# Performance work log

Hardware: AMD Instinct MI355X
Metric: run time of the kernel (lower is better)

## Reference

```python
import jax, jax.numpy as jnp
import numpy as np

B, T, D = 256, 512, 8      # batch, seq_len, Feature_number
H = 120                    # hidden_size
L = 4                      # layers=['s','s','s','s']
NH = D                     # num_heads = Feature_number
HD = H // NH               # head dim = 15
EPS = 1e-5


def setup_inputs() -> dict:
    key = jax.random.key(0)
    ks = jax.random.split(key, 16)
    rn = lambda k, shape, s=0.1: (jax.random.normal(k, shape, jnp.float32) * s)
    return {
        "x":   jax.random.normal(ks[0], (B, T, D), jnp.float32),
        # input->gate weights, stacked over layers
        "Wi":  rn(ks[1], (L, H, D)),
        "Wf":  rn(ks[2], (L, H, D)),
        "Wz":  rn(ks[3], (L, H, D)),
        "Wo":  rn(ks[4], (L, H, D)),
        # block-diagonal (multi-head) recurrent weights: [L, NH, HD, HD]
        "Ri":  rn(ks[5], (L, NH, HD, HD)),
        "Rf":  rn(ks[6], (L, NH, HD, HD)),
        "Rz":  rn(ks[7], (L, NH, HD, HD)),
        "Ro":  rn(ks[8], (L, NH, HD, HD)),
        "bi":  rn(ks[9],  (L, H), 0.02),
        "bf":  rn(ks[10], (L, H), 0.02),
        "bz":  rn(ks[11], (L, H), 0.02),
        "bo":  rn(ks[12], (L, H), 0.02),
        # per-block down-projection back to Feature_number (residual block)
        "Wp":  rn(ks[13], (L, D, H)),
        "bp":  jnp.zeros((L, D), jnp.float32),
        # BatchNorm1d(Feature_number) affine params
        "gamma": jnp.ones((D,), jnp.float32),
        "beta":  jnp.zeros((D,), jnp.float32),
        # fc5: Linear(Feature_number, 1)
        "Wfc": rn(ks[14], (1, D)),
        "bfc": jnp.zeros((1,), jnp.float32),
    }


def _slstm_layer(x, Wi, Wf, Wz, Wo, Ri, Rf, Rz, Ro, bi, bf, bz, bo, Wp, bp):
    """One sLSTM block: exp-gated recurrence with stabilizer, then down-proj + residual.
    x: [B, T, D] -> [B, T, D]."""
    Bn = x.shape[0]

    def rec(h, R):  # block-diagonal recurrent matmul: [B,H] x [NH,HD,HD] -> [B,H]
        return jnp.einsum("bnd,nde->bne", h.reshape(Bn, NH, HD), R).reshape(Bn, H)

    def step(carry, x_t):
        h, c, n, m = carry                       # each [B, H]
        it = x_t @ Wi.T + rec(h, Ri) + bi        # input gate pre-act
        ft = x_t @ Wf.T + rec(h, Rf) + bf        # forget gate pre-act (exp gating)
        z = jnp.tanh(x_t @ Wz.T + rec(h, Rz) + bz)
        o = jax.nn.sigmoid(x_t @ Wo.T + rec(h, Ro) + bo)
        m_new = jnp.maximum(ft + m, it)          # stabilizer state
        i_p = jnp.exp(it - m_new)
        f_p = jnp.exp(ft + m - m_new)
        c_new = f_p * c + i_p * z
        n_new = f_p * n + i_p                    # normalizer state
        h_new = o * (c_new / n_new)
        return (h_new, c_new, n_new, m_new), h_new

    z0 = jnp.zeros((Bn, H), x.dtype)
    (_, _, _, _), hs = jax.lax.scan(step, (z0, z0, z0, z0), jnp.swapaxes(x, 0, 1))
    y = jnp.einsum("tbh,dh->tbd", hs, Wp) + bp   # down-project to D
    return x + jnp.swapaxes(y, 0, 1)             # residual


def reference(x, Wi, Wf, Wz, Wo, Ri, Rf, Rz, Ro, bi, bf, bz, bo, Wp, bp,
              gamma, beta, Wfc, bfc):
    h = x
    for l in range(L):
        h = _slstm_layer(h, Wi[l], Wf[l], Wz[l], Wo[l], Ri[l], Rf[l], Rz[l], Ro[l],
                         bi[l], bf[l], bz[l], bo[l], Wp[l], bp[l])
    last = h[:, -1, :]                            # [B, D]
    # BatchNorm1d in training mode (batch stats, biased variance)
    mu = jnp.mean(last, axis=0)
    var = jnp.mean((last - mu) ** 2, axis=0)
    bn = (last - mu) / jnp.sqrt(var + EPS) * gamma + beta
    out = jax.nn.sigmoid(bn @ Wfc.T + bfc)        # [B, 1]
    return out[:, 0]                              # squeeze(1) -> [B]
```

## Files before the change

### kernel.cpp

```cpp
#include <hip/hip_runtime.h>
#include <math.h>

#define Bsz 256
#define T   512
#define Dd  8
#define Hh  120
#define Ll  4
#define NHn 8
#define HDd 15
#define HP  16
#define EPSf 1e-5f

__device__ __forceinline__ float fast_rcp(float x) {
#if __has_builtin(__builtin_amdgcn_rcpf)
    return __builtin_amdgcn_rcpf(x);
#else
    return 1.f / x;
#endif
}
__device__ __forceinline__ float tanh_fast(float x) {
    float e = __expf(2.f * x);
    return 1.f - 2.f * fast_rcp(e + 1.f);
}
__device__ __forceinline__ float sigm_fast(float x) {
    return fast_rcp(1.f + __expf(-x));
}

__global__ __launch_bounds__(512, 2) void slstm_kernel(
    const float* __restrict__ x,
    const float* __restrict__ Wi, const float* __restrict__ Wf,
    const float* __restrict__ Wz, const float* __restrict__ Wo,
    const float* __restrict__ Ri, const float* __restrict__ Rf,
    const float* __restrict__ Rz, const float* __restrict__ Ro,
    const float* __restrict__ bi, const float* __restrict__ bf,
    const float* __restrict__ bz, const float* __restrict__ bo,
    const float* __restrict__ Wp, const float* __restrict__ bp,
    float* __restrict__ last_out)
{
    __shared__ __align__(16) float xs[T * Dd];
    __shared__ __align__(16) float hb[Ll][2][NHn * HP];

    const int tid = threadIdx.x;
    const int b   = blockIdx.x;
    const int l   = tid >> 7;
    const int j   = tid & 127;

    {
        const float4* xg  = (const float4*)(x + (size_t)b * T * Dd);
        float4*       xs4 = (float4*)xs;
        xs4[tid]       = xg[tid];
        xs4[tid + 512] = xg[tid + 512];
        ((float*)hb)[tid]       = 0.f;
        ((float*)hb)[tid + 512] = 0.f;
    }

    const bool gl = (j < Hh);
    const int jj  = gl ? j : 0;
    const int n   = jj / HDd;
    const int e   = jj - n * HDd;
    float wI[Dd], wF[Dd], wZ[Dd], wO[Dd];
    float rI[HDd], rF[HDd], rZ[HDd], rO[HDd];
    {
        const int row = (l * Hh + jj) * Dd;
#pragma unroll
        for (int d = 0; d < Dd; ++d) {
            wI[d] = Wi[row + d]; wF[d] = Wf[row + d];
            wZ[d] = Wz[row + d]; wO[d] = Wo[row + d];
        }
        const int rb = ((l * NHn + n) * HDd) * HDd + e;
#pragma unroll
        for (int d = 0; d < HDd; ++d) {
            rI[d] = Ri[rb + d * HDd]; rF[d] = Rf[rb + d * HDd];
            rZ[d] = Rz[rb + d * HDd]; rO[d] = Ro[rb + d * HDd];
        }
    }
    float bI = bi[l * Hh + jj], bF = bf[l * Hh + jj];
    float bZ = bz[l * Hh + jj], bO = bo[l * Hh + jj];

    const int p  = (j >= 64) ? (j - 64) : j;
    const int d8 = p & 7, ch = p >> 3;
    float wp_r[16];
    {
        const int base = l * Dd * Hh + d8 * Hh + ch * HDd;
#pragma unroll
        for (int k = 0; k < HDd; ++k) wp_r[k] = Wp[base + k];
        wp_r[15] = 0.f;
    }
    float bp_r = bp[l * Dd + d8];

#pragma unroll
    for (int d = 0; d < Dd; ++d)
        asm volatile("" : "+v"(wI[d]), "+v"(wF[d]), "+v"(wZ[d]), "+v"(wO[d]));
#pragma unroll
    for (int d = 0; d < HDd; ++d)
        asm volatile("" : "+v"(rI[d]), "+v"(rF[d]), "+v"(rZ[d]), "+v"(rO[d]));
#pragma unroll
    for (int k = 0; k < 16; ++k)
        asm volatile("" : "+v"(wp_r[k]));
    asm volatile("" : "+v"(bI), "+v"(bF), "+v"(bZ), "+v"(bO));
    asm volatile("" : "+v"(bp_r));

    float cst = 0.f, nst = 0.f, mst = 0.f;

    __syncthreads();

    for (int tau = 0; tau < T + 2 * Ll - 1; ++tau) {
        const int t_g = tau - 2 * l;
        const int t_p = t_g - 1;

        if (gl && (t_g >= 0) && (t_g < T)) {
            const float4* xt4 = (const float4*)(xs + t_g * Dd);
            const float4 xa = xt4[0], xb2 = xt4[1];
            const float xv[Dd] = {xa.x, xa.y, xa.z, xa.w, xb2.x, xb2.y, xb2.z, xb2.w};
            float gi = bI, gf = bF, gz = bZ, go = bO;
#pragma unroll
            for (int d = 0; d < Dd; ++d) {
                gi = fmaf(xv[d], wI[d], gi);
                gf = fmaf(xv[d], wF[d], gf);
                gz = fmaf(xv[d], wZ[d], gz);
                go = fmaf(xv[d], wO[d], go);
            }
            const float4* h4 = (const float4*)(&hb[l][t_g & 1][n * HP]);
            const float4 h0 = h4[0], h1 = h4[1], h2 = h4[2], h3 = h4[3];
            const float hv[16] = {h0.x, h0.y, h0.z, h0.w, h1.x, h1.y, h1.z, h1.w,
                                  h2.x, h2.y, h2.z, h2.w, h3.x, h3.y, h3.z, h3.w};
#pragma unroll
            for (int d = 0; d < HDd; ++d) {
                gi = fmaf(hv[d], rI[d], gi);
                gf = fmaf(hv[d], rF[d], gf);
                gz = fmaf(hv[d], rZ[d], gz);
                go = fmaf(hv[d], rO[d], go);
            }
            const float z  = tanh_fast(gz);
            const float o  = sigm_fast(go);
            const float mn = fmaxf(gf + mst, gi);
            const float ip = __expf(gi - mn);
            const float fp = __expf(gf + mst - mn);
            cst = fmaf(fp, cst, ip * z);
            nst = fmaf(fp, nst, ip);
            mst = mn;
            const float hnew = o * cst * fast_rcp(nst);
            hb[l][(t_g & 1) ^ 1][n * HP + e] = hnew;
        }

        if ((j >= 64) && (t_p >= 0) && (t_p < T)) {
            const float4* h4 = (const float4*)(&hb[l][t_g & 1][ch * HP]);
            const float4 h0 = h4[0], h1 = h4[1], h2 = h4[2], h3 = h4[3];
            const float hv[16] = {h0.x, h0.y, h0.z, h0.w, h1.x, h1.y, h1.z, h1.w,
                                  h2.x, h2.y, h2.z, h2.w, h3.x, h3.y, h3.z, h3.w};
            float s = 0.f;
#pragma unroll
            for (int k = 0; k < 16; ++k) s = fmaf(hv[k], wp_r[k], s);
            s += __shfl_xor(s, 8);
            s += __shfl_xor(s, 16);
            s += __shfl_xor(s, 32);
            if (p < Dd) xs[t_p * Dd + p] += s + bp_r;
        }

        __syncthreads();
    }

    if (tid < Dd) last_out[b * Dd + tid] = xs[(T - 1) * Dd + tid];
}

__global__ __launch_bounds__(Bsz) void bn_fc_kernel(
    const float* __restrict__ last,
    const float* __restrict__ gamma, const float* __restrict__ beta,
    const float* __restrict__ Wfc,   const float* __restrict__ bfc,
    float* __restrict__ out)
{
    __shared__ float ls[Bsz][Dd];
    __shared__ float mu[Dd], rstdg[Dd], bet[Dd], wfc[Dd];
    const int tid = threadIdx.x;
#pragma unroll
    for (int d = 0; d < Dd; ++d) ls[tid][d] = last[tid * Dd + d];
    __syncthreads();
    if (tid < Dd) {
        float s = 0.f;
        for (int bb = 0; bb < Bsz; ++bb) s += ls[bb][tid];
        const float mean = s * (1.f / Bsz);
        float v = 0.f;
        for (int bb = 0; bb < Bsz; ++bb) {
            const float dd = ls[bb][tid] - mean;
            v += dd * dd;
        }
        v *= (1.f / Bsz);
        mu[tid]    = mean;
        rstdg[tid] = rsqrtf(v + EPSf) * gamma[tid];
        bet[tid]   = beta[tid];
        wfc[tid]   = Wfc[tid];
    }
    __syncthreads();
    float acc = bfc[0];
#pragma unroll
    for (int d = 0; d < Dd; ++d)
        acc += ((ls[tid][d] - mu[d]) * rstdg[d] + bet[d]) * wfc[d];
    out[tid] = sigm_fast(acc);
}

extern "C" void kernel_launch(void* const* d_in, const int* in_sizes, int n_in,
                              void* d_out, int out_size, void* d_ws, size_t ws_size,
                              hipStream_t stream) {
    const float* x    = (const float*)d_in[0];
    const float* Wi   = (const float*)d_in[1];
    const float* Wf   = (const float*)d_in[2];
    const float* Wz   = (const float*)d_in[3];
    const float* Wo   = (const float*)d_in[4];
    const float* Ri   = (const float*)d_in[5];
    const float* Rf   = (const float*)d_in[6];
    const float* Rz   = (const float*)d_in[7];
    const float* Ro   = (const float*)d_in[8];
    const float* bi   = (const float*)d_in[9];
    const float* bf   = (const float*)d_in[10];
    const float* bz   = (const float*)d_in[11];
    const float* bo   = (const float*)d_in[12];
    const float* Wp   = (const float*)d_in[13];
    const float* bp   = (const float*)d_in[14];
    const float* gamma= (const float*)d_in[15];
    const float* beta = (const float*)d_in[16];
    const float* Wfc  = (const float*)d_in[17];
    const float* bfc  = (const float*)d_in[18];

    float* last_ws = (float*)d_ws;
    float* out     = (float*)d_out;

    slstm_kernel<<<Bsz, 512, 0, stream>>>(x, Wi, Wf, Wz, Wo, Ri, Rf, Rz, Ro,
                                          bi, bf, bz, bo, Wp, bp, last_ws);
    bn_fc_kernel<<<1, Bsz, 0, stream>>>(last_ws, gamma, beta, Wfc, bfc, out);
}
```

Baseline: 453.1 us.

## Pad hidden-state rows, pin weights in loop, parallelize BN reduction

```diff
diff --git a/kernel.cpp b/kernel.cpp
--- a/kernel.cpp
+++ b/kernel.cpp
@@ -8,7 +8,7 @@
 #define Ll  4
 #define NHn 8
 #define HDd 15
-#define HP  16
+#define HP  20
 #define EPSf 1e-5f
 
 __device__ __forceinline__ float fast_rcp(float x) {
@@ -50,8 +50,10 @@
         float4*       xs4 = (float4*)xs;
         xs4[tid]       = xg[tid];
         xs4[tid + 512] = xg[tid + 512];
-        ((float*)hb)[tid]       = 0.f;
-        ((float*)hb)[tid + 512] = 0.f;
+        float* hbf = (float*)hb;
+        hbf[tid]       = 0.f;
+        hbf[tid + 512] = 0.f;
+        if (tid < 256) hbf[tid + 1024] = 0.f;
     }
 
     const bool gl = (j < Hh);
@@ -88,23 +90,22 @@
     }
     float bp_r = bp[l * Dd + d8];
 
-#pragma unroll
-    for (int d = 0; d < Dd; ++d)
-        asm volatile("" : "+v"(wI[d]), "+v"(wF[d]), "+v"(wZ[d]), "+v"(wO[d]));
-#pragma unroll
-    for (int d = 0; d < HDd; ++d)
-        asm volatile("" : "+v"(rI[d]), "+v"(rF[d]), "+v"(rZ[d]), "+v"(rO[d]));
-#pragma unroll
-    for (int k = 0; k < 16; ++k)
-        asm volatile("" : "+v"(wp_r[k]));
-    asm volatile("" : "+v"(bI), "+v"(bF), "+v"(bZ), "+v"(bO));
-    asm volatile("" : "+v"(bp_r));
-
     float cst = 0.f, nst = 0.f, mst = 0.f;
 
     __syncthreads();
 
     for (int tau = 0; tau < T + 2 * Ll - 1; ++tau) {
+#pragma unroll
+        for (int d = 0; d < Dd; ++d)
+            asm volatile("" : "+v"(wI[d]), "+v"(wF[d]), "+v"(wZ[d]), "+v"(wO[d]));
+#pragma unroll
+        for (int d = 0; d < HDd; ++d)
+            asm volatile("" : "+v"(rI[d]), "+v"(rF[d]), "+v"(rZ[d]), "+v"(rO[d]));
+#pragma unroll
+        for (int k = 0; k < 16; k += 4)
+            asm volatile("" : "+v"(wp_r[k]), "+v"(wp_r[k+1]), "+v"(wp_r[k+2]), "+v"(wp_r[k+3]));
+        asm volatile("" : "+v"(bI), "+v"(bF), "+v"(bZ), "+v"(bO), "+v"(bp_r));
+
         const int t_g = tau - 2 * l;
         const int t_p = t_g - 1;
 
@@ -139,8 +140,7 @@
             cst = fmaf(fp, cst, ip * z);
             nst = fmaf(fp, nst, ip);
             mst = mn;
-            const float hnew = o * cst * fast_rcp(nst);
-            hb[l][(t_g & 1) ^ 1][n * HP + e] = hnew;
+            hb[l][(t_g & 1) ^ 1][n * HP + e] = o * cst * fast_rcp(nst);
         }
 
         if ((j >= 64) && (t_p >= 0) && (t_p < T)) {
@@ -169,24 +169,35 @@
     const float* __restrict__ Wfc,   const float* __restrict__ bfc,
     float* __restrict__ out)
 {
-    __shared__ float ls[Bsz][Dd];
+    __shared__ __align__(16) float ls[Bsz][Dd];
+    __shared__ float rsum[32][Dd], rsq[32][Dd];
     __shared__ float mu[Dd], rstdg[Dd], bet[Dd], wfc[Dd];
     const int tid = threadIdx.x;
-#pragma unroll
-    for (int d = 0; d < Dd; ++d) ls[tid][d] = last[tid * Dd + d];
+    {
+        const float4* lg = (const float4*)last;
+        ((float4*)ls)[tid]       = lg[tid];
+        ((float4*)ls)[tid + 256] = lg[tid + 256];
+    }
+    __syncthreads();
+    {
+        const int d = tid & 7, g = tid >> 3;
+        float s = 0.f, q = 0.f;
+#pragma unroll
+        for (int k = 0; k < 8; ++k) {
+            const float v = ls[g + 32 * k][d];
+            s += v; q = fmaf(v, v, q);
+        }
+        rsum[g][d] = s; rsq[g][d] = q;
+    }
     __syncthreads();
     if (tid < Dd) {
-        float s = 0.f;
-        for (int bb = 0; bb < Bsz; ++bb) s += ls[bb][tid];
+        float s = 0.f, q = 0.f;
+#pragma unroll
+        for (int g = 0; g < 32; ++g) { s += rsum[g][tid]; q += rsq[g][tid]; }
         const float mean = s * (1.f / Bsz);
-        float v = 0.f;
-        for (int bb = 0; bb < Bsz; ++bb) {
-            const float dd = ls[bb][tid] - mean;
-            v += dd * dd;
-        }
-        v *= (1.f / Bsz);
+        const float var  = q * (1.f / Bsz) - mean * mean;
         mu[tid]    = mean;
-        rstdg[tid] = rsqrtf(v + EPSf) * gamma[tid];
+        rstdg[tid] = rsqrtf(fmaxf(var, 0.f) + EPSf) * gamma[tid];
         bet[tid]   = beta[tid];
         wfc[tid]   = Wfc[tid];
     }
```

Result: slower. 467.3 us (+3.1%).
